# Kernel tuning notes

Hardware: AMD Instinct MI355X
Metric: run time of the kernel (lower is better)

## Reference

```python
import jax, jax.numpy as jnp
import numpy as np

FSAMPLE = 100.0


def _butter_sos(N, Wn, btype):
    """Butterworth digital SOS design (bilinear transform), matching scipy.signal.butter
    up to section ordering (same transfer function)."""
    fs = 2.0
    k = np.arange(1, N + 1)
    p = np.exp(1j * np.pi * (2 * k + N - 1) / (2 * N))  # analog prototype poles, gain 1
    if btype == 'low':
        warped = 2 * fs * np.tan(np.pi * float(Wn) / fs)
        p = p * warped
        z = np.array([], dtype=complex)
        gain = warped ** N
    else:  # bandpass
        w1 = 2 * fs * np.tan(np.pi * Wn[0] / fs)
        w2 = 2 * fs * np.tan(np.pi * Wn[1] / fs)
        bw = w2 - w1
        wo = np.sqrt(w1 * w2)
        plp = p * bw / 2.0
        disc = np.sqrt(plp ** 2 - wo ** 2)
        p = np.concatenate([plp + disc, plp - disc])
        z = np.zeros(N, dtype=complex)
        gain = bw ** N
    fs2 = 2 * fs
    gain = gain * np.real(np.prod(fs2 - z) / np.prod(fs2 - p))
    pd = (fs2 + p) / (fs2 - p)            # bilinear-transformed poles
    # digital zeros: mapped analog zeros plus padding zeros at z=-1
    # lowpass -> all zeros at -1 -> b = [1,2,1]; bandpass -> zeros at +1 and -1 -> b = [1,0,-1]
    b_proto = np.array([1.0, 2.0, 1.0]) if btype == 'low' else np.array([1.0, 0.0, -1.0])
    pp = pd[np.imag(pd) > 0]              # one pole per conjugate pair
    rows = []
    for i, pi in enumerate(pp):
        a = np.array([1.0, -2.0 * np.real(pi), np.abs(pi) ** 2])
        b = b_proto * (gain if i == 0 else 1.0)
        rows.append(np.concatenate([b, a]))
    return np.stack(rows).astype(np.float32)  # [n_sections, 6]


def _biquad(w, b, a):
    """Direct-form I biquad along time. w: [NC, T]; b, a: length-3 (a[0] may != 1)."""
    b = b / a[0]
    a = a / a[0]

    def step(carry, xn):  # xn: [NC]
        x1, x2, y1, y2 = carry
        y = b[0] * xn + b[1] * x1 + b[2] * x2 - a[1] * y1 - a[2] * y2
        return (xn, x1, y, y1), y

    z = jnp.zeros_like(w[:, 0])
    _, ys = jax.lax.scan(step, (z, z, z, z), w.T)  # ys: [T, NC]
    return ys.T


def _sosfilt(w, sos):
    for i in range(sos.shape[0]):  # small fixed number of sections
        w = _biquad(w, sos[i, :3], sos[i, 3:])
    return w


def setup_inputs() -> dict:
    key = jax.random.key(0)
    B, T, C = 16, 16384, 64
    x = jax.random.normal(key, (B, T, C), dtype=jnp.float32)
    nyq = FSAMPLE / 2.0
    bp_sos = jnp.asarray(_butter_sos(2, [6.0 / nyq, 20.0 / nyq], 'band'))
    lp_sos = jnp.asarray(_butter_sos(4, 10.0 / nyq, 'low'))
    return {"x": x, "bp_sos": bp_sos, "lp_sos": lp_sos}


def reference(x, bp_sos, lp_sos):
    B, T, C = x.shape
    w = jnp.transpose(x, (0, 2, 1)).reshape(B * C, T)  # filter along time
    w = _sosfilt(w, bp_sos)          # bandpass 6-20 Hz
    w = _sosfilt(w * w, lp_sos)      # square then lowpass 10 Hz
    return jnp.transpose(w.reshape(B, C, T), (0, 2, 1))
```

## Files before the change

kernel.cpp:

```cpp
#include <hip/hip_runtime.h>

#define B_LEN 16
#define T_LEN 16384
#define C_LEN 64
#define CHUNK 64
#define WARM  64

__global__ __launch_bounds__(256) void iir_chunked_kernel(
    const float* __restrict__ x,
    const float* __restrict__ bp,
    const float* __restrict__ lp,
    float* __restrict__ out)
{
    const int c     = threadIdx.x & 63;
    const int bsub  = threadIdx.x >> 6;
    const int b     = blockIdx.y * 4 + bsub;
    const int chunk = blockIdx.x;

    const float b10 = bp[0], b11 = bp[1], b12 = bp[2],  a11 = -bp[4],  a12 = -bp[5];
    const float b20 = bp[6], b21 = bp[7], b22 = bp[8],  a21 = -bp[10], a22 = -bp[11];
    const float b30 = lp[0], b31 = lp[1], b32 = lp[2],  a31 = -lp[4],  a32 = -lp[5];
    const float b40 = lp[6], b41 = lp[7], b42 = lp[8],  a41 = -lp[10], a42 = -lp[11];

    const int t_out0 = chunk * CHUNK;
    const int warm   = (t_out0 < WARM) ? t_out0 : WARM;
    const int t0     = t_out0 - warm;

    float s11 = 0.f, s12 = 0.f;
    float s21 = 0.f, s22 = 0.f;
    float s31 = 0.f, s32 = 0.f;
    float s41 = 0.f, s42 = 0.f;

    int idx = (b * T_LEN + t0) * C_LEN + c;

    auto step = [&](float xn) -> float {
        float y1 = fmaf(b10, xn, s11);
        s11 = fmaf(b11, xn, fmaf(a11, y1, s12));
        s12 = fmaf(b12, xn, a12 * y1);
        float y2 = fmaf(b20, y1, s21);
        s21 = fmaf(b21, y1, fmaf(a21, y2, s22));
        s22 = fmaf(b22, y1, a22 * y2);
        float v = y2 * y2;
        float y3 = fmaf(b30, v, s31);
        s31 = fmaf(b31, v, fmaf(a31, y3, s32));
        s32 = fmaf(b32, v, a32 * y3);
        float y4 = fmaf(b40, y3, s41);
        s41 = fmaf(b41, y3, fmaf(a41, y4, s42));
        s42 = fmaf(b42, y3, a42 * y4);
        return y4;
    };

#pragma unroll 8
    for (int i = 0; i < warm; ++i) {
        float xn = x[idx];
        idx += C_LEN;
        step(xn);
    }
#pragma unroll 8
    for (int i = 0; i < CHUNK; ++i) {
        float xn = x[idx];
        out[idx] = step(xn);
        idx += C_LEN;
    }
}

extern "C" void kernel_launch(void* const* d_in, const int* in_sizes, int n_in,
                              void* d_out, int out_size, void* d_ws, size_t ws_size,
                              hipStream_t stream) {
    const float* x  = (const float*)d_in[0];
    const float* bp = (const float*)d_in[1];
    const float* lp = (const float*)d_in[2];
    float* out      = (float*)d_out;

    dim3 grid(T_LEN / CHUNK, B_LEN / 4);
    dim3 block(256);
    iir_chunked_kernel<<<grid, block, 0, stream>>>(x, bp, lp, out);
}
```

Before: 127.4 us.

## Software-pipeline input loads with rotating register buffers and nontemporal stores

Replaces the plain per-sample load/compute loops with a four-buffer register prefetch scheme. Each buffer holds 8 time steps, so up to 32 samples of loads are in flight while the serial biquad recurrence runs on earlier data. Output writes become nontemporal stores to reduce cache pollution. This raises register pressure and fully unrolls the code, which may lower occupancy or increase instruction-cache footprint.

```diff
diff --git a/kernel.cpp b/kernel.cpp
--- a/kernel.cpp
+++ b/kernel.cpp
@@ -6,7 +6,7 @@
 #define CHUNK 64
 #define WARM  64
 
-__global__ __launch_bounds__(256) void iir_chunked_kernel(
+__global__ __launch_bounds__(256) void iir_pipe_kernel(
     const float* __restrict__ x,
     const float* __restrict__ bp,
     const float* __restrict__ lp,
@@ -31,7 +31,8 @@
     float s31 = 0.f, s32 = 0.f;
     float s41 = 0.f, s42 = 0.f;
 
-    int idx = (b * T_LEN + t0) * C_LEN + c;
+    const float* __restrict__ lq = x   + ((size_t)b * T_LEN + t0)     * C_LEN + c;
+    float*       __restrict__ po = out + ((size_t)b * T_LEN + t_out0) * C_LEN + c;
 
     auto step = [&](float xn) -> float {
         float y1 = fmaf(b10, xn, s11);
@@ -50,18 +51,43 @@
         return y4;
     };
 
-#pragma unroll 8
-    for (int i = 0; i < warm; ++i) {
-        float xn = x[idx];
-        idx += C_LEN;
-        step(xn);
+    float P0[8], P1[8], P2[8], P3[8];
+
+    auto load8 = [&](float* d) {
+#pragma unroll
+        for (int j = 0; j < 8; ++j) d[j] = lq[j * C_LEN];
+        lq += 8 * C_LEN;
+    };
+    auto warm8 = [&](const float* d) {
+#pragma unroll
+        for (int j = 0; j < 8; ++j) step(d[j]);
+    };
+    auto emit8 = [&](const float* d) {
+#pragma unroll
+        for (int j = 0; j < 8; ++j) {
+            float y = step(d[j]);
+            __builtin_nontemporal_store(y, po);
+            po += C_LEN;
+        }
+    };
+
+    load8(P0); load8(P1); load8(P2); load8(P3);
+
+    const int nrot = warm >> 5;
+    for (int r = 0; r < nrot; ++r) {
+        warm8(P0); load8(P0);
+        warm8(P1); load8(P1);
+        warm8(P2); load8(P2);
+        warm8(P3); load8(P3);
     }
-#pragma unroll 8
-    for (int i = 0; i < CHUNK; ++i) {
-        float xn = x[idx];
-        out[idx] = step(xn);
-        idx += C_LEN;
-    }
+    emit8(P0); load8(P0);
+    emit8(P1); load8(P1);
+    emit8(P2); load8(P2);
+    emit8(P3); load8(P3);
+    emit8(P0);
+    emit8(P1);
+    emit8(P2);
+    emit8(P3);
 }
 
 extern "C" void kernel_launch(void* const* d_in, const int* in_sizes, int n_in,
@@ -74,5 +100,5 @@
 
     dim3 grid(T_LEN / CHUNK, B_LEN / 4);
     dim3 block(256);
-    iir_chunked_kernel<<<grid, block, 0, stream>>>(x, bp, lp, out);
+    iir_pipe_kernel<<<grid, block, 0, stream>>>(x, bp, lp, out);
 }
```

Result: faster. 119.1 us (-6.4%).

## Process four channels per thread with vec4 loads and register-prefetched pipeline

Applied to the files above, without the earlier changes.

Each thread now filters four adjacent channels, so the four recurrence chains run side by side for instruction-level parallelism. Inputs and outputs move as 16-byte vectors, and stores are nontemporal. A rotating set of four 16-step register buffers prefetches the next time steps while the current ones are filtered, with sched barriers fixing the order. The grid shrinks to one block per time chunk covering all batches. This lowers wave count and occupancy, so overlap relies on the explicit prefetch and the independent chains.

```diff
diff --git a/kernel.cpp b/kernel.cpp
--- a/kernel.cpp
+++ b/kernel.cpp
@@ -6,15 +6,16 @@
 #define CHUNK 64
 #define WARM  64
 
-__global__ __launch_bounds__(256) void iir_chunked_kernel(
+typedef float f32x4 __attribute__((ext_vector_type(4)));
+
+__global__ __launch_bounds__(256, 1) void iir_vec4_kernel(
     const float* __restrict__ x,
     const float* __restrict__ bp,
     const float* __restrict__ lp,
     float* __restrict__ out)
 {
-    const int c     = threadIdx.x & 63;
-    const int bsub  = threadIdx.x >> 6;
-    const int b     = blockIdx.y * 4 + bsub;
+    const int cq    = threadIdx.x & 15;
+    const int b     = threadIdx.x >> 4;
     const int chunk = blockIdx.x;
 
     const float b10 = bp[0], b11 = bp[1], b12 = bp[2],  a11 = -bp[4],  a12 = -bp[5];
@@ -26,42 +27,98 @@
     const int warm   = (t_out0 < WARM) ? t_out0 : WARM;
     const int t0     = t_out0 - warm;
 
-    float s11 = 0.f, s12 = 0.f;
-    float s21 = 0.f, s22 = 0.f;
-    float s31 = 0.f, s32 = 0.f;
-    float s41 = 0.f, s42 = 0.f;
+    float s11[4] = {0,0,0,0}, s12[4] = {0,0,0,0};
+    float s21[4] = {0,0,0,0}, s22[4] = {0,0,0,0};
+    float s31[4] = {0,0,0,0}, s32[4] = {0,0,0,0};
+    float s41[4] = {0,0,0,0}, s42[4] = {0,0,0,0};
 
-    int idx = (b * T_LEN + t0) * C_LEN + c;
+    const float* __restrict__ lq = x   + ((size_t)b * T_LEN + t0)     * C_LEN + 4 * cq;
+    float*       __restrict__ po = out + ((size_t)b * T_LEN + t_out0) * C_LEN + 4 * cq;
 
-    auto step = [&](float xn) -> float {
-        float y1 = fmaf(b10, xn, s11);
-        s11 = fmaf(b11, xn, fmaf(a11, y1, s12));
-        s12 = fmaf(b12, xn, a12 * y1);
-        float y2 = fmaf(b20, y1, s21);
-        s21 = fmaf(b21, y1, fmaf(a21, y2, s22));
-        s22 = fmaf(b22, y1, a22 * y2);
-        float v = y2 * y2;
-        float y3 = fmaf(b30, v, s31);
-        s31 = fmaf(b31, v, fmaf(a31, y3, s32));
-        s32 = fmaf(b32, v, a32 * y3);
-        float y4 = fmaf(b40, y3, s41);
-        s41 = fmaf(b41, y3, fmaf(a41, y4, s42));
-        s42 = fmaf(b42, y3, a42 * y4);
-        return y4;
+    auto step4 = [&](const float* xn4, float* y4) {
+#pragma unroll
+        for (int ch = 0; ch < 4; ++ch) {
+            float xn = xn4[ch];
+            float y1 = fmaf(b10, xn, s11[ch]);
+            s11[ch] = fmaf(b11, xn, fmaf(a11, y1, s12[ch]));
+            s12[ch] = fmaf(b12, xn, a12 * y1);
+            float y2 = fmaf(b20, y1, s21[ch]);
+            s21[ch] = fmaf(b21, y1, fmaf(a21, y2, s22[ch]));
+            s22[ch] = fmaf(b22, y1, a22 * y2);
+            float v = y2 * y2;
+            float y3 = fmaf(b30, v, s31[ch]);
+            s31[ch] = fmaf(b31, v, fmaf(a31, y3, s32[ch]));
+            s32[ch] = fmaf(b32, v, a32 * y3);
+            float y4v = fmaf(b40, y3, s41[ch]);
+            s41[ch] = fmaf(b41, y3, fmaf(a41, y4v, s42[ch]));
+            s42[ch] = fmaf(b42, y3, a42 * y4v);
+            y4[ch] = y4v;
+        }
     };
 
-#pragma unroll 8
-    for (int i = 0; i < warm; ++i) {
-        float xn = x[idx];
-        idx += C_LEN;
-        step(xn);
+    float P0[16], P1[16], P2[16], P3[16];
+
+    auto load4 = [&](float* d) {
+#pragma unroll
+        for (int j = 0; j < 4; ++j)
+            *reinterpret_cast<f32x4*>(d + 4 * j) =
+                *reinterpret_cast<const f32x4*>(lq + j * C_LEN);
+        lq += 4 * C_LEN;
+    };
+    auto warm4 = [&](float* d) {
+        float yt[4];
+#pragma unroll
+        for (int j = 0; j < 4; ++j) step4(d + 4 * j, yt);
+    };
+    auto fence = [&]() { __builtin_amdgcn_sched_barrier(0); };
+
+    auto emit4_reload = [&](float* d) {
+        float Y[16];
+#pragma unroll
+        for (int j = 0; j < 4; ++j) step4(d + 4 * j, Y + 4 * j);
+        load4(d);
+        fence();
+#pragma unroll
+        for (int j = 0; j < 4; ++j)
+            __builtin_nontemporal_store(*reinterpret_cast<const f32x4*>(Y + 4 * j),
+                                        reinterpret_cast<f32x4*>(po + j * C_LEN));
+        po += 4 * C_LEN;
+        fence();
+    };
+    auto emit4_final = [&](float* d) {
+        float Y[16];
+#pragma unroll
+        for (int j = 0; j < 4; ++j) step4(d + 4 * j, Y + 4 * j);
+#pragma unroll
+        for (int j = 0; j < 4; ++j)
+            __builtin_nontemporal_store(*reinterpret_cast<const f32x4*>(Y + 4 * j),
+                                        reinterpret_cast<f32x4*>(po + j * C_LEN));
+        po += 4 * C_LEN;
+        fence();
+    };
+
+    load4(P0); load4(P1); load4(P2); load4(P3);
+    fence();
+
+    const int nrot = warm >> 4;
+#pragma unroll 1
+    for (int r = 0; r < nrot; ++r) {
+        warm4(P0); load4(P0); fence();
+        warm4(P1); load4(P1); fence();
+        warm4(P2); load4(P2); fence();
+        warm4(P3); load4(P3); fence();
     }
-#pragma unroll 8
-    for (int i = 0; i < CHUNK; ++i) {
-        float xn = x[idx];
-        out[idx] = step(xn);
-        idx += C_LEN;
+#pragma unroll 1
+    for (int r = 0; r < (CHUNK - 16) / 16; ++r) {
+        emit4_reload(P0);
+        emit4_reload(P1);
+        emit4_reload(P2);
+        emit4_reload(P3);
     }
+    emit4_final(P0);
+    emit4_final(P1);
+    emit4_final(P2);
+    emit4_final(P3);
 }
 
 extern "C" void kernel_launch(void* const* d_in, const int* in_sizes, int n_in,
@@ -72,7 +129,7 @@
     const float* lp = (const float*)d_in[2];
     float* out      = (float*)d_out;
 
-    dim3 grid(T_LEN / CHUNK, B_LEN / 4);
+    dim3 grid(T_LEN / CHUNK);
     dim3 block(256);
-    iir_chunked_kernel<<<grid, block, 0, stream>>>(x, bp, lp, out);
+    iir_vec4_kernel<<<grid, block, 0, stream>>>(x, bp, lp, out);
 }
```

Result: faster. 118.7 us (-6.8%).

## Software-pipeline global loads with inline asm ring buffer and explicit vmcnt waits

Applied to the files above, without the earlier changes.

Replaces the simple per-sample load loop with a four-deep ring of eight-sample register batches. The batches are loaded with inline global_load_dword asm and consumed after explicit s_waitcnt vmcnt waits, so memory latency overlaps the serial IIR recurrence. The warm-up and output phases are fully unrolled, and the vmcnt thresholds are hand-tuned to count interleaved stores. It also adds an occupancy hint to the launch bounds. The cost is fragile hand-written waitcnt accounting and higher register pressure.

```diff
diff --git a/kernel.cpp b/kernel.cpp
--- a/kernel.cpp
+++ b/kernel.cpp
@@ -6,7 +6,29 @@
 #define CHUNK 64
 #define WARM  64
 
-__global__ __launch_bounds__(256) void iir_chunked_kernel(
+
+#define LOADG(g) do {                                                     \
+    asm volatile(                                                         \
+        "global_load_dword %0, %8, off\n\t"                               \
+        "global_load_dword %1, %8, off offset:256\n\t"                    \
+        "global_load_dword %2, %8, off offset:512\n\t"                    \
+        "global_load_dword %3, %8, off offset:768\n\t"                    \
+        "global_load_dword %4, %8, off offset:1024\n\t"                   \
+        "global_load_dword %5, %8, off offset:1280\n\t"                   \
+        "global_load_dword %6, %8, off offset:1536\n\t"                   \
+        "global_load_dword %7, %8, off offset:1792\n\t"                   \
+        : "=&v"((g)[0]), "=&v"((g)[1]), "=&v"((g)[2]), "=&v"((g)[3]),     \
+          "=&v"((g)[4]), "=&v"((g)[5]), "=&v"((g)[6]), "=&v"((g)[7])      \
+        : "v"(lq) : "memory");                                            \
+    lq += 8 * C_LEN;                                                      \
+} while (0)
+
+#define WAITV(n) do {                                                     \
+    asm volatile("s_waitcnt vmcnt(" #n ")" ::: "memory");                 \
+    __builtin_amdgcn_sched_barrier(0);                                    \
+} while (0)
+
+__global__ __launch_bounds__(256, 4) void iir_asm_kernel(
     const float* __restrict__ x,
     const float* __restrict__ bp,
     const float* __restrict__ lp,
@@ -31,7 +53,8 @@
     float s31 = 0.f, s32 = 0.f;
     float s41 = 0.f, s42 = 0.f;
 
-    int idx = (b * T_LEN + t0) * C_LEN + c;
+    const float* lq = x   + ((size_t)b * T_LEN + t0)     * C_LEN + c;
+    float*       po = out + ((size_t)b * T_LEN + t_out0) * C_LEN + c;
 
     auto step = [&](float xn) -> float {
         float y1 = fmaf(b10, xn, s11);
@@ -50,18 +73,37 @@
         return y4;
     };
 
-#pragma unroll 8
-    for (int i = 0; i < warm; ++i) {
-        float xn = x[idx];
-        idx += C_LEN;
-        step(xn);
+    float P[4][8];
+
+    LOADG(P[0]); LOADG(P[1]); LOADG(P[2]); LOADG(P[3]);
+
+    if (warm) {
+#pragma unroll
+        for (int i = 0; i < 8; ++i) {
+            WAITV(24);
+#pragma unroll
+            for (int j = 0; j < 8; ++j) step(P[i & 3][j]);
+            LOADG(P[i & 3]);
+        }
     }
-#pragma unroll 8
-    for (int i = 0; i < CHUNK; ++i) {
-        float xn = x[idx];
-        out[idx] = step(xn);
-        idx += C_LEN;
-    }
+
+#define EMIT_PHASE(K, N, DOLOAD) do {                                     \
+        WAITV(N);                                                         \
+        _Pragma("unroll")                                                 \
+        for (int j = 0; j < 8; ++j)                                       \
+            po[(K * 8 + j) * C_LEN] = step(P[K & 3][j]);                  \
+        if (DOLOAD) LOADG(P[K & 3]);                                      \
+    } while (0)
+
+    EMIT_PHASE(0, 24, 1);
+    EMIT_PHASE(1, 32, 1);
+    EMIT_PHASE(2, 40, 1);
+    EMIT_PHASE(3, 48, 1);
+    EMIT_PHASE(4, 48, 0);
+    EMIT_PHASE(5, 40, 0);
+    EMIT_PHASE(6, 32, 0);
+    EMIT_PHASE(7, 24, 0);
+#undef EMIT_PHASE
 }
 
 extern "C" void kernel_launch(void* const* d_in, const int* in_sizes, int n_in,
@@ -74,5 +116,5 @@
 
     dim3 grid(T_LEN / CHUNK, B_LEN / 4);
     dim3 block(256);
-    iir_chunked_kernel<<<grid, block, 0, stream>>>(x, bp, lp, out);
+    iir_asm_kernel<<<grid, block, 0, stream>>>(x, bp, lp, out);
 }
```

After: 122.8 us. 1.04x faster.
